# Optimization experiments

Measured on AMD Instinct MI355X. Metric: run time of the kernel, lower is better.

## Reference

```python
import jax, jax.numpy as jnp
import numpy as np

EPS = 1e-08  # matches torch default eps in both F.normalize and PairwiseDistance


def setup_inputs() -> dict:
    key = jax.random.key(0)
    x = jax.random.normal(key, (8192, 1024), dtype=jnp.float32)
    return {"x": x}


def reference(x) -> jnp.ndarray:
    B = x.shape[0]
    # F.normalize(x, p=2, dim=-1, eps=EPS): x / max(||x||_2, eps)
    norms = jnp.linalg.norm(x, axis=-1, keepdims=True)
    xn = x / jnp.maximum(norms, EPS)
    # cosine similarity matrix [B, B]
    cos_sim = xn @ xn.T
    # fill_diagonal_(-2): exclude self from nearest-neighbor search
    idx = jnp.arange(B)
    cos_sim = cos_sim.at[idx, idx].set(-2.0)
    nn_idx = jnp.argmax(cos_sim, axis=1)  # [B] int
    # torch PairwiseDistance(p=2, eps=EPS): ||x1 - x2 + eps||_2
    diff = xn - xn[nn_idx] + EPS
    nn_dist = jnp.sqrt(jnp.sum(diff * diff, axis=-1))  # [B]
    loss = -jnp.mean(jnp.log(nn_dist + EPS))
    return loss
```

## Files before the change

kernel.cpp:

```cpp
#include <hip/hip_runtime.h>
#include <hip/hip_bf16.h>
#include <math.h>

#define NB 8192
#define ND 1024
#define KEPS 1e-8f
#define SLOTS 128

typedef __attribute__((ext_vector_type(8))) __bf16 bf16x8;
typedef __attribute__((ext_vector_type(4))) float f32x4;

__device__ __forceinline__ unsigned int fmono(float f) {
    unsigned int b = __float_as_uint(f);
    return b ^ ((b & 0x80000000u) ? 0xFFFFFFFFu : 0x80000000u);
}

__device__ __forceinline__ unsigned short f2bf(float f) {
    union { float f; unsigned int u; } a;
    a.f = f;
    unsigned int lsb = (a.u >> 16) & 1u;
    a.u += 0x7fffu + lsb;
    return (unsigned short)(a.u >> 16);
}

__device__ __forceinline__ void gload_lds16(const void* g, void* l) {
    __builtin_amdgcn_global_load_lds(
        (const __attribute__((address_space(1))) unsigned int*)g,
        (__attribute__((address_space(3))) unsigned int*)l, 16, 0, 0);
}

__global__ __launch_bounds__(256) void normalize_k(const float* __restrict__ x,
                                                   unsigned short* __restrict__ xnb) {
    int row = blockIdx.x;
    int t = threadIdx.x;
    float4 v = ((const float4*)(x + (size_t)row * ND))[t];
    float ss = v.x * v.x + v.y * v.y + v.z * v.z + v.w * v.w;
#pragma unroll
    for (int off = 32; off > 0; off >>= 1) ss += __shfl_down(ss, off, 64);
    __shared__ float sred[4];
    if ((t & 63) == 0) sred[t >> 6] = ss;
    __syncthreads();
    float tot = sred[0] + sred[1] + sred[2] + sred[3];
    float scale = 1.0f / fmaxf(sqrtf(tot), KEPS);
    ushort4 o;
    o.x = f2bf(v.x * scale);
    o.y = f2bf(v.y * scale);
    o.z = f2bf(v.z * scale);
    o.w = f2bf(v.w * scale);
    ((ushort4*)xnb)[(size_t)row * (ND / 4) + t] = o;
}

__global__ __launch_bounds__(256) void argmax_gemm(const unsigned short* __restrict__ xnb,
                                                   unsigned long long* __restrict__ partial) {
    const int bx = blockIdx.x, by = blockIdx.y;
    if (bx < by) return;

    __shared__ unsigned short As[128 * 32];
    __shared__ unsigned short Bs[128 * 32];

    const int tid = threadIdx.x;
    const int w = tid >> 6;
    const int l = tid & 63;
    const int wM = w >> 1;
    const int wN = w & 1;
    const int rowBase = by * 128, colBase = bx * 128;

    f32x4 acc[4][4];
#pragma unroll
    for (int m = 0; m < 4; ++m)
#pragma unroll
        for (int n = 0; n < 4; ++n) acc[m][n] = f32x4{0.f, 0.f, 0.f, 0.f};

    const int lr = l >> 2;
    const int lc = (l & 3) * 8;
    const int lm = l & 15;
    const int ko = (l >> 4) * 8;

    for (int kk = 0; kk < ND; kk += 32) {
#pragma unroll
        for (int q = 0; q < 2; ++q) {
            int rl = (w * 2 + q) * 16 + lr;
            gload_lds16(xnb + (size_t)(rowBase + rl) * ND + kk + lc, &As[(w * 2 + q) * 512]);
            gload_lds16(xnb + (size_t)(colBase + rl) * ND + kk + lc, &Bs[(w * 2 + q) * 512]);
        }
        __syncthreads();

        bf16x8 af[4], bf[4];
#pragma unroll
        for (int m = 0; m < 4; ++m)
            af[m] = *(const bf16x8*)&As[(wM * 64 + m * 16 + lm) * 32 + ko];
#pragma unroll
        for (int n = 0; n < 4; ++n)
            bf[n] = *(const bf16x8*)&Bs[(wN * 64 + n * 16 + lm) * 32 + ko];
#pragma unroll
        for (int m = 0; m < 4; ++m)
#pragma unroll
            for (int n = 0; n < 4; ++n)
                acc[m][n] = __builtin_amdgcn_mfma_f32_16x16x32_bf16(af[m], bf[n], acc[m][n], 0, 0, 0);
        __syncthreads();
    }

#pragma unroll
    for (int m = 0; m < 4; ++m) {
#pragma unroll
        for (int r = 0; r < 4; ++r) {
            int gi = rowBase + wM * 64 + m * 16 + (l >> 4) * 4 + r;
            float mx = -3.0f;
            int mc = 0x7FFFFFFF;
#pragma unroll
            for (int n = 0; n < 4; ++n) {
                int gj = colBase + wN * 64 + n * 16 + lm;
                float v = (gi == gj) ? -2.0f : acc[m][n][r];
                if (v > mx) { mx = v; mc = gj; }
            }
#pragma unroll
            for (int off = 1; off < 16; off <<= 1) {
                float omx = __shfl_xor(mx, off, 64);
                int omc = __shfl_xor(mc, off, 64);
                if (omx > mx || (omx == mx && omc < mc)) { mx = omx; mc = omc; }
            }
            if (lm == 0) {
                unsigned long long p = ((unsigned long long)fmono(mx) << 32) |
                                       (unsigned long long)(~(unsigned int)mc);
                partial[(size_t)gi * SLOTS + bx * 2 + wN] = p;
            }
        }
    }

    if (bx > by) {
#pragma unroll
        for (int n = 0; n < 4; ++n) {
            int gj = colBase + wN * 64 + n * 16 + lm;
            float mx = -3.0f;
            int mc = 0x7FFFFFFF;
#pragma unroll
            for (int m = 0; m < 4; ++m) {
#pragma unroll
                for (int r = 0; r < 4; ++r) {
                    int gi = rowBase + wM * 64 + m * 16 + (l >> 4) * 4 + r;
                    float v = (gi == gj) ? -2.0f : acc[m][n][r];
                    if (v > mx) { mx = v; mc = gi; }
                }
            }
#pragma unroll
            for (int off = 16; off < 64; off <<= 1) {
                float omx = __shfl_xor(mx, off, 64);
                int omc = __shfl_xor(mc, off, 64);
                if (omx > mx || (omx == mx && omc < mc)) { mx = omx; mc = omc; }
            }
            if ((l >> 4) == 0) {
                unsigned long long p = ((unsigned long long)fmono(mx) << 32) |
                                       (unsigned long long)(~(unsigned int)mc);
                partial[(size_t)gj * SLOTS + by * 2 + wM] = p;
            }
        }
    }
}

__global__ __launch_bounds__(256) void dist_k(const float* __restrict__ x,
                                              const unsigned long long* __restrict__ partial,
                                              float* __restrict__ rowloss) {
    int i = blockIdx.x;
    int t = threadIdx.x;
    unsigned long long p = 0ull;
    if (t < SLOTS) p = partial[(size_t)i * SLOTS + t];
#pragma unroll
    for (int off = 1; off < 64; off <<= 1) {
        unsigned long long o = __shfl_xor(p, off, 64);
        if (o > p) p = o;
    }
    __shared__ unsigned long long sp[4];
    __shared__ int sj;
    if ((t & 63) == 0) sp[t >> 6] = p;
    __syncthreads();
    if (t == 0) {
        unsigned long long b = sp[0];
        for (int k = 1; k < 4; ++k)
            if (sp[k] > b) b = sp[k];
        sj = (int)(~(unsigned int)(b & 0xFFFFFFFFull));
    }
    __syncthreads();
    int j = sj;

    float4 a = ((const float4*)(x + (size_t)i * ND))[t];
    float4 b = ((const float4*)(x + (size_t)j * ND))[t];
    float sa = a.x * a.x + a.y * a.y + a.z * a.z + a.w * a.w;
    float sb = b.x * b.x + b.y * b.y + b.z * b.z + b.w * b.w;
#pragma unroll
    for (int off = 32; off > 0; off >>= 1) {
        sa += __shfl_down(sa, off, 64);
        sb += __shfl_down(sb, off, 64);
    }
    __shared__ float sra[4], srb[4];
    if ((t & 63) == 0) { sra[t >> 6] = sa; srb[t >> 6] = sb; }
    __syncthreads();
    float na = sra[0] + sra[1] + sra[2] + sra[3];
    float nb = srb[0] + srb[1] + srb[2] + srb[3];
    float ia = 1.0f / fmaxf(sqrtf(na), KEPS);
    float ib = 1.0f / fmaxf(sqrtf(nb), KEPS);
    float dx = a.x * ia - b.x * ib + KEPS;
    float dy = a.y * ia - b.y * ib + KEPS;
    float dz = a.z * ia - b.z * ib + KEPS;
    float dw = a.w * ia - b.w * ib + KEPS;
    float ss = dx * dx + dy * dy + dz * dz + dw * dw;
#pragma unroll
    for (int off = 32; off > 0; off >>= 1) ss += __shfl_down(ss, off, 64);
    __shared__ float srd[4];
    if ((t & 63) == 0) srd[t >> 6] = ss;
    __syncthreads();
    if (t == 0) {
        float tot = srd[0] + srd[1] + srd[2] + srd[3];
        rowloss[i] = -logf(sqrtf(tot) + KEPS);
    }
}

__global__ __launch_bounds__(1024) void reduce_k(const float* __restrict__ rowloss,
                                                 float* __restrict__ out) {
    int t = threadIdx.x;
    float s = 0.0f;
#pragma unroll
    for (int k = 0; k < 8; ++k) s += rowloss[t + k * 1024];
#pragma unroll
    for (int off = 32; off > 0; off >>= 1) s += __shfl_down(s, off, 64);
    __shared__ float sred[16];
    if ((t & 63) == 0) sred[t >> 6] = s;
    __syncthreads();
    if (t == 0) {
        float tot = 0.0f;
        for (int k = 0; k < 16; ++k) tot += sred[k];
        out[0] = tot / (float)NB;
    }
}

extern "C" void kernel_launch(void* const* d_in, const int* in_sizes, int n_in,
                              void* d_out, int out_size, void* d_ws, size_t ws_size,
                              hipStream_t stream) {
    const float* x = (const float*)d_in[0];
    float* out = (float*)d_out;

    char* ws = (char*)d_ws;
    unsigned short* xnb = (unsigned short*)ws;
    unsigned long long* partial =
        (unsigned long long*)(ws + (size_t)NB * ND * 2);
    float* rowloss = (float*)(ws + (size_t)NB * ND * 2 + (size_t)NB * SLOTS * 8);

    normalize_k<<<NB, 256, 0, stream>>>(x, xnb);
    argmax_gemm<<<dim3(NB / 128, NB / 128), 256, 0, stream>>>(xnb, partial);
    dist_k<<<NB, 256, 0, stream>>>(x, partial, rowloss);
    reduce_k<<<1, 1024, 0, stream>>>(rowloss, out);
}
```

Baseline: 222.9 us.

## Rewrite argmax GEMM with 256x256 tiles, double-buffered LDS, compact triangular grid

Replaces the 128x128 tile GEMM, which launched a full 64x64 grid and exited the lower half, with a 1D grid of 528 upper-triangular 256x256 tiles run by 512 threads. Global loads go straight into LDS and are double-buffered over 128KB of dynamic shared memory with XOR swizzles. Staged prefetches are interleaved with MFMA quarters under s_setprio, and the tile index is remapped across XCDs. The partial slot layout and the dist_k slot count change to match. The cost is heavy register and LDS pressure from the larger tiles, plus more complex slot indexing.

```diff
diff --git a/kernel.cpp b/kernel.cpp
--- a/kernel.cpp
+++ b/kernel.cpp
@@ -6,6 +6,9 @@
 #define ND 1024
 #define KEPS 1e-8f
 #define SLOTS 128
+#define NTILE 32
+#define NWG 528
+#define NKT 16
 
 typedef __attribute__((ext_vector_type(8))) __bf16 bf16x8;
 typedef __attribute__((ext_vector_type(4))) float f32x4;
@@ -14,7 +17,6 @@
     unsigned int b = __float_as_uint(f);
     return b ^ ((b & 0x80000000u) ? 0xFFFFFFFFu : 0x80000000u);
 }
-
 __device__ __forceinline__ unsigned short f2bf(float f) {
     union { float f; unsigned int u; } a;
     a.f = f;
@@ -22,11 +24,14 @@
     a.u += 0x7fffu + lsb;
     return (unsigned short)(a.u >> 16);
 }
-
 __device__ __forceinline__ void gload_lds16(const void* g, void* l) {
     __builtin_amdgcn_global_load_lds(
         (const __attribute__((address_space(1))) unsigned int*)g,
         (__attribute__((address_space(3))) unsigned int*)l, 16, 0, 0);
+}
+__device__ __forceinline__ unsigned long long packmax(float mx, int mc) {
+    return ((unsigned long long)fmono(mx) << 32) |
+           (unsigned long long)(~(unsigned int)mc);
 }
 
 __global__ __launch_bounds__(256) void normalize_k(const float* __restrict__ x,
@@ -50,66 +55,111 @@
     ((ushort4*)xnb)[(size_t)row * (ND / 4) + t] = o;
 }
 
-__global__ __launch_bounds__(256) void argmax_gemm(const unsigned short* __restrict__ xnb,
-                                                   unsigned long long* __restrict__ partial) {
-    const int bx = blockIdx.x, by = blockIdx.y;
-    if (bx < by) return;
-
-    __shared__ unsigned short As[128 * 32];
-    __shared__ unsigned short Bs[128 * 32];
-
-    const int tid = threadIdx.x;
-    const int w = tid >> 6;
+#define FENCE_BARRIER() do { asm volatile("" ::: "memory"); \
+    __builtin_amdgcn_s_barrier(); asm volatile("" ::: "memory"); } while (0)
+#define WAIT_VM2() asm volatile("s_waitcnt vmcnt(2)" ::: "memory")
+#define WAIT_VM0() asm volatile("s_waitcnt vmcnt(0)" ::: "memory")
+
+#define STAGE_HALF(H, DBB) do { \
+    gload_lds16(sp[H][0], ldsb + (DBB) + ((H) >> 1) * 32768 + ((H) & 1) * 16384 + (0 * 8 + wv) * 1024); \
+    gload_lds16(sp[H][1], ldsb + (DBB) + ((H) >> 1) * 32768 + ((H) & 1) * 16384 + (1 * 8 + wv) * 1024); \
+    sp[H][0] += 128; sp[H][1] += 128; } while (0)
+
+#define LOAD_A(MH) do { \
+    const char* Ab_ = ldsb + cbB + wM * 16384 + laneA; \
+    _Pragma("unroll") for (int mi = 0; mi < 4; ++mi) \
+    _Pragma("unroll") for (int ks = 0; ks < 2; ++ks) \
+        af[mi][ks] = *(const bf16x8*)(Ab_ + ((((MH) * 4 + mi) * 2 + ks) * 1024)); } while (0)
+
+#define LOAD_B(BANK, NH) do { \
+    const char* Bb_ = ldsb + cbB + 32768 + (wN >> 1) * 16384 + laneA; \
+    _Pragma("unroll") for (int ni = 0; ni < 2; ++ni) \
+    _Pragma("unroll") for (int ks = 0; ks < 2; ++ks) \
+        BANK[ni][ks] = *(const bf16x8*)(Bb_ + ((((wN & 1) * 4 + (NH) * 2 + ni) * 2 + ks) * 1024)); } while (0)
+
+#define MFMAQ(MH, NH, BANK) do { \
+    __builtin_amdgcn_s_setprio(1); \
+    _Pragma("unroll") for (int mi = 0; mi < 4; ++mi) \
+    _Pragma("unroll") for (int ni = 0; ni < 2; ++ni) { \
+        acc[(MH) * 4 + mi][(NH) * 2 + ni] = __builtin_amdgcn_mfma_f32_16x16x32_bf16( \
+            af[mi][0], BANK[ni][0], acc[(MH) * 4 + mi][(NH) * 2 + ni], 0, 0, 0); \
+        acc[(MH) * 4 + mi][(NH) * 2 + ni] = __builtin_amdgcn_mfma_f32_16x16x32_bf16( \
+            af[mi][1], BANK[ni][1], acc[(MH) * 4 + mi][(NH) * 2 + ni], 0, 0, 0); } \
+    __builtin_amdgcn_s_setprio(0); } while (0)
+
+__global__ __launch_bounds__(512, 2) void argmax_gemm(const unsigned short* __restrict__ xnb,
+                                                      unsigned long long* __restrict__ partial) {
+    extern __shared__ char ldsb[];
+
+    int wg = (int)blockIdx.x;
+    int tile = (wg & 7) * (NWG / 8) + (wg >> 3);
+    int by = 0, tr = tile;
+    while (tr >= NTILE - by) { tr -= NTILE - by; ++by; }
+    const int bx = by + tr;
+
+    const int rowBase = by * 256, colBase = bx * 256;
+    const int tid = (int)threadIdx.x;
+    const int wv = tid >> 6;
     const int l = tid & 63;
-    const int wM = w >> 1;
-    const int wN = w & 1;
-    const int rowBase = by * 128, colBase = bx * 128;
-
-    f32x4 acc[4][4];
-#pragma unroll
-    for (int m = 0; m < 4; ++m)
+    const int wM = wv >> 2;
+    const int wN = wv & 3;
+
+    const int laneA = (l & 15) * 64 + (((l >> 4) * 16) ^ ((l & 8) << 2));
+
+    const int scb = ((l & 3) * 16) ^ ((l >> 5) << 5);
+    const int srow = (l >> 2) & 15;
+
+    const char* xb = (const char*)xnb;
+    const char* sp[4][2];
+#pragma unroll
+    for (int h = 0; h < 4; ++h)
+#pragma unroll
+        for (int q = 0; q < 2; ++q) {
+            int s = q * 8 + wv;
+            int rgrp = s >> 1, kgrp = s & 1;
+            int panel = (h >> 1) ? colBase : rowBase;
+            long long grow = panel + (h & 1) * 128 + rgrp * 16 + srow;
+            sp[h][q] = xb + grow * (ND * 2) + kgrp * 64 + scb;
+        }
+
+    f32x4 acc[8][4];
+#pragma unroll
+    for (int m = 0; m < 8; ++m)
 #pragma unroll
         for (int n = 0; n < 4; ++n) acc[m][n] = f32x4{0.f, 0.f, 0.f, 0.f};
 
-    const int lr = l >> 2;
-    const int lc = (l & 3) * 8;
-    const int lm = l & 15;
-    const int ko = (l >> 4) * 8;
-
-    for (int kk = 0; kk < ND; kk += 32) {
-#pragma unroll
-        for (int q = 0; q < 2; ++q) {
-            int rl = (w * 2 + q) * 16 + lr;
-            gload_lds16(xnb + (size_t)(rowBase + rl) * ND + kk + lc, &As[(w * 2 + q) * 512]);
-            gload_lds16(xnb + (size_t)(colBase + rl) * ND + kk + lc, &Bs[(w * 2 + q) * 512]);
-        }
-        __syncthreads();
-
-        bf16x8 af[4], bf[4];
-#pragma unroll
-        for (int m = 0; m < 4; ++m)
-            af[m] = *(const bf16x8*)&As[(wM * 64 + m * 16 + lm) * 32 + ko];
-#pragma unroll
-        for (int n = 0; n < 4; ++n)
-            bf[n] = *(const bf16x8*)&Bs[(wN * 64 + n * 16 + lm) * 32 + ko];
-#pragma unroll
-        for (int m = 0; m < 4; ++m)
-#pragma unroll
-            for (int n = 0; n < 4; ++n)
-                acc[m][n] = __builtin_amdgcn_mfma_f32_16x16x32_bf16(af[m], bf[n], acc[m][n], 0, 0, 0);
-        __syncthreads();
-    }
-
-#pragma unroll
-    for (int m = 0; m < 4; ++m) {
+    STAGE_HALF(0, 0); STAGE_HALF(1, 0); STAGE_HALF(2, 0); STAGE_HALF(3, 0);
+
+    int cbB = 0, dbB = 65536;
+    for (int c = 0; c < NKT; ++c) {
+        const bool pf = (c + 1 < NKT);
+        bf16x8 af[4][2], b0[2][2], b1[2][2];
+        if (pf) { STAGE_HALF(0, dbB); WAIT_VM2(); } else { WAIT_VM0(); }
+        FENCE_BARRIER();
+        LOAD_A(0); LOAD_B(b0, 0);
+        MFMAQ(0, 0, b0);
+        if (pf) STAGE_HALF(1, dbB);
+        LOAD_B(b1, 1);
+        MFMAQ(0, 1, b1);
+        if (pf) STAGE_HALF(2, dbB);
+        LOAD_A(1);
+        MFMAQ(1, 1, b1);
+        if (pf) STAGE_HALF(3, dbB);
+        MFMAQ(1, 0, b0);
+        FENCE_BARRIER();
+        int tmp = cbB; cbB = dbB; dbB = tmp;
+    }
+
+#pragma unroll
+    for (int m = 0; m < 8; ++m) {
 #pragma unroll
         for (int r = 0; r < 4; ++r) {
-            int gi = rowBase + wM * 64 + m * 16 + (l >> 4) * 4 + r;
+            int gi = rowBase + wM * 128 + m * 16 + (l >> 4) * 4 + r;
             float mx = -3.0f;
             int mc = 0x7FFFFFFF;
 #pragma unroll
             for (int n = 0; n < 4; ++n) {
-                int gj = colBase + wN * 64 + n * 16 + lm;
+                int gj = colBase + wN * 64 + n * 16 + (l & 15);
                 float v = (gi == gj) ? -2.0f : acc[m][n][r];
                 if (v > mx) { mx = v; mc = gj; }
             }
@@ -119,25 +169,21 @@
                 int omc = __shfl_xor(mc, off, 64);
                 if (omx > mx || (omx == mx && omc < mc)) { mx = omx; mc = omc; }
             }
-            if (lm == 0) {
-                unsigned long long p = ((unsigned long long)fmono(mx) << 32) |
-                                       (unsigned long long)(~(unsigned int)mc);
-                partial[(size_t)gi * SLOTS + bx * 2 + wN] = p;
-            }
+            if ((l & 15) == 0)
+                partial[(size_t)gi * SLOTS + (2 * by + (bx - by) * 4 + wN)] = packmax(mx, mc);
         }
     }
-
     if (bx > by) {
 #pragma unroll
         for (int n = 0; n < 4; ++n) {
-            int gj = colBase + wN * 64 + n * 16 + lm;
+            int gj = colBase + wN * 64 + n * 16 + (l & 15);
             float mx = -3.0f;
             int mc = 0x7FFFFFFF;
 #pragma unroll
-            for (int m = 0; m < 4; ++m) {
+            for (int m = 0; m < 8; ++m) {
 #pragma unroll
                 for (int r = 0; r < 4; ++r) {
-                    int gi = rowBase + wM * 64 + m * 16 + (l >> 4) * 4 + r;
+                    int gi = rowBase + wM * 128 + m * 16 + (l >> 4) * 4 + r;
                     float v = (gi == gj) ? -2.0f : acc[m][n][r];
                     if (v > mx) { mx = v; mc = gi; }
                 }
@@ -148,11 +194,8 @@
                 int omc = __shfl_xor(mc, off, 64);
                 if (omx > mx || (omx == mx && omc < mc)) { mx = omx; mc = omc; }
             }
-            if ((l >> 4) == 0) {
-                unsigned long long p = ((unsigned long long)fmono(mx) << 32) |
-                                       (unsigned long long)(~(unsigned int)mc);
-                partial[(size_t)gj * SLOTS + by * 2 + wM] = p;
-            }
+            if ((l >> 4) == 0)
+                partial[(size_t)gj * SLOTS + (2 * by + wM)] = packmax(mx, mc);
         }
     }
 }
@@ -162,21 +205,22 @@
                                               float* __restrict__ rowloss) {
     int i = blockIdx.x;
     int t = threadIdx.x;
+    int nv = SLOTS - 2 * (i >> 8);
     unsigned long long p = 0ull;
-    if (t < SLOTS) p = partial[(size_t)i * SLOTS + t];
+    if (t < nv) p = partial[(size_t)i * SLOTS + t];
 #pragma unroll
     for (int off = 1; off < 64; off <<= 1) {
         unsigned long long o = __shfl_xor(p, off, 64);
         if (o > p) p = o;
     }
-    __shared__ unsigned long long sp[4];
+    __shared__ unsigned long long sp_[4];
     __shared__ int sj;
-    if ((t & 63) == 0) sp[t >> 6] = p;
+    if ((t & 63) == 0) sp_[t >> 6] = p;
     __syncthreads();
     if (t == 0) {
-        unsigned long long b = sp[0];
+        unsigned long long b = sp_[0];
         for (int k = 1; k < 4; ++k)
-            if (sp[k] > b) b = sp[k];
+            if (sp_[k] > b) b = sp_[k];
         sj = (int)(~(unsigned int)(b & 0xFFFFFFFFull));
     }
     __syncthreads();
@@ -244,8 +288,11 @@
         (unsigned long long*)(ws + (size_t)NB * ND * 2);
     float* rowloss = (float*)(ws + (size_t)NB * ND * 2 + (size_t)NB * SLOTS * 8);
 
+    (void)hipFuncSetAttribute((const void*)argmax_gemm,
+                              hipFuncAttributeMaxDynamicSharedMemorySize, 131072);
+
     normalize_k<<<NB, 256, 0, stream>>>(x, xnb);
-    argmax_gemm<<<dim3(NB / 128, NB / 128), 256, 0, stream>>>(xnb, partial);
+    argmax_gemm<<<NWG, 512, 131072, stream>>>(xnb, partial);
     dist_k<<<NB, 256, 0, stream>>>(x, partial, rowloss);
     reduce_k<<<1, 1024, 0, stream>>>(rowloss, out);
 }
```

Measured after the change: 209.6 us. -6.0%, faster.
